# Kernel tuning notes

Hardware: AMD Instinct MI355X
Metric: run time of the kernel (lower is better)

## Reference

```python
import jax, jax.numpy as jnp
import numpy as np

B, N_GENES, N_SETS, G = 256, 10000, 1000, 128   # batch, input_dim, output_dim, geneset_size
H1, H2 = 64, 32                                  # hidden_dims
EPS = 1e-5                                       # BatchNorm1d eps


def _batchnorm(h, gamma, beta):
    # BatchNorm1d in training mode: biased batch stats over the batch axis
    mean = jnp.mean(h, axis=0, keepdims=True)
    var = jnp.mean(jnp.square(h - mean), axis=0, keepdims=True)
    return (h - mean) * jax.lax.rsqrt(var + EPS) * gamma + beta


def setup_inputs() -> dict:
    key = jax.random.key(0)
    ks = jax.random.split(key, 7)
    # Adjacency with exactly G distinct ones per column -> gather index list [N_SETS, G]
    rng = np.random.default_rng(0)
    gene_idx = np.argsort(rng.random((N_SETS, N_GENES)), axis=1)[:, :G]
    gene_idx = jnp.asarray(np.sort(gene_idx, axis=1), dtype=jnp.int32)

    x = jax.random.normal(ks[0], (B, N_GENES), jnp.float32)
    s1, s2, s3 = 1.0 / np.sqrt(G), 1.0 / np.sqrt(H1), 1.0 / np.sqrt(H2)
    W1 = jax.random.uniform(ks[1], (N_SETS, G, H1), jnp.float32, -s1, s1)
    b1 = jax.random.uniform(ks[2], (N_SETS, H1), jnp.float32, -s1, s1)
    W2 = jax.random.uniform(ks[3], (N_SETS, H1, H2), jnp.float32, -s2, s2)
    b2 = jax.random.uniform(ks[4], (N_SETS, H2), jnp.float32, -s2, s2)
    W3 = jax.random.uniform(ks[5], (N_SETS, H2), jnp.float32, -s3, s3)
    b3 = jax.random.uniform(ks[6], (N_SETS,), jnp.float32, -s3, s3)
    g1 = jnp.ones((N_SETS, H1), jnp.float32)
    be1 = jnp.zeros((N_SETS, H1), jnp.float32)
    g2 = jnp.ones((N_SETS, H2), jnp.float32)
    be2 = jnp.zeros((N_SETS, H2), jnp.float32)
    return {"x": x, "gene_idx": gene_idx, "W1": W1, "b1": b1, "g1": g1, "be1": be1,
            "W2": W2, "b2": b2, "g2": g2, "be2": be2, "W3": W3, "b3": b3}


def reference(x, gene_idx, W1, b1, g1, be1, W2, b2, g2, be2, W3, b3):
    # Per-geneset gather: x[:, adj[:,i]==1] for all i at once -> [B, S, G]
    xg = x[:, gene_idx]
    # Linear -> ReLU -> BatchNorm (per geneset, grouped GEMM)
    h = jax.nn.relu(jnp.einsum('bsg,sgh->bsh', xg, W1) + b1)
    h = _batchnorm(h, g1, be1)
    h = jax.nn.relu(jnp.einsum('bsh,shk->bsk', h, W2) + b2)
    h = _batchnorm(h, g2, be2)
    # Final Linear(H2 -> 1) -> ReLU, concatenated over genesets -> [B, S]
    out = jax.nn.relu(jnp.einsum('bsh,sh->bs', h, W3) + b3)
    return out
```

## Files before the change

### kernel.cpp

```cpp
#include <hip/hip_runtime.h>
#include <hip/hip_bf16.h>
#include <stdint.h>

#define BB 256
#define NG 10000
#define NS 1000
#define GG 128
#define H1 64
#define H2 32
#define EPSV 1e-5f


typedef unsigned short ushortT;
typedef __attribute__((ext_vector_type(4))) short short4v;
typedef __attribute__((ext_vector_type(8))) short short8v;
typedef __attribute__((ext_vector_type(4))) float float4v;

__device__ __forceinline__ float bf2f(ushortT u) {
    union { uint32_t i; float f; } v; v.i = ((uint32_t)u) << 16; return v.f;
}
__device__ __forceinline__ ushortT f2bf(float f) {
    union { __hip_bfloat16 h; ushortT u; } cv;
    cv.h = __float2bfloat16(f);
    return cv.u;
}
__device__ __forceinline__ uint32_t pack2(ushortT lo, ushortT hi) {
    return (uint32_t)lo | ((uint32_t)hi << 16);
}
__device__ __forceinline__ bool probe_f32(const void* g1) {
    return ((*(const uint32_t*)g1) & 0xFFFFu) == 0u;
}
__device__ __forceinline__ float loadf(const void* p, int i, bool isf) {
    return isf ? ((const float*)p)[i] : bf2f(((const ushortT*)p)[i]);
}
__device__ __forceinline__ ushortT loadbf(const void* p, size_t i, bool isf) {
    return isf ? f2bf(((const float*)p)[i]) : ((const ushortT*)p)[i];
}

__global__ __launch_bounds__(256) void k_transpose(const void* __restrict__ x,
                                                   ushortT* __restrict__ xT,
                                                   const void* __restrict__ g1p) {
    __shared__ ushortT tile[64][66];
    const bool isf = probe_f32(g1p);
    const int tx = threadIdx.x & 63;
    const int tz = threadIdx.x >> 6;
    const int j0 = blockIdx.x * 64;
    const int b0 = blockIdx.y * 64;
    const int j = j0 + tx;
#pragma unroll
    for (int k = 0; k < 16; ++k) {
        int bl = tz * 16 + k;
        ushortT v = 0;
        if (j < NG) v = loadbf(x, (size_t)(b0 + bl) * NG + j, isf);
        tile[bl][tx] = v;
    }
    __syncthreads();
#pragma unroll
    for (int k = 0; k < 16; ++k) {
        int jl = tz * 16 + k;
        int jw = j0 + jl;
        if (jw < NG) xT[jw * BB + b0 + tx] = tile[tx][jl];
    }
}

__global__ __launch_bounds__(256, 3) void k_main(
    const ushortT* __restrict__ xT, const int* __restrict__ gidx,
    const void* __restrict__ W1, const void* __restrict__ W2,
    const void* __restrict__ b1, const void* __restrict__ g1, const void* __restrict__ be1,
    const void* __restrict__ b2, const void* __restrict__ g2, const void* __restrict__ be2,
    const void* __restrict__ W3, const void* __restrict__ b3,
    void* __restrict__ out) {
    __shared__ ushortT xg[BB * 68];
    __shared__ ushortT w1s[2][64 * 36];

    char* xgc = (char*)xg;
    float* redf = (float*)w1s;
    ushortT* w2s = (ushortT*)w1s;

    const bool isf = probe_f32(g1);
    const int s = blockIdx.x;
    const int t = threadIdx.x;
    const int w = t >> 6;
    const int lane = t & 63;
    const int l16 = lane & 15;
    const int quad = lane >> 4;
    const size_t base1 = (size_t)s * (GG * H1);
    const size_t base2 = (size_t)s * (H1 * H2);

#define HOLEI(i)     (*(int*)(xgc + ((i) >> 1) * 136 + 128 + ((i) & 1) * 4))
#define HOLEF(r0, k) (*(float*)(xgc + ((r0) + ((k) >> 1)) * 136 + 128 + ((k) & 1) * 4))

    float b1v[4], w3v[2], b2v[2];
#pragma unroll
    for (int nt = 0; nt < 4; ++nt) b1v[nt] = loadf(b1, s * H1 + nt * 16 + l16, isf);
#pragma unroll
    for (int nt = 0; nt < 2; ++nt) {
        b2v[nt] = loadf(b2, s * H2 + nt * 16 + l16, isf);
        w3v[nt] = loadf(W3, s * H2 + nt * 16 + l16, isf);
    }
    const float b3v = loadf(b3, s, isf);
    float g1v = 0.f, be1v = 0.f, g2v = 0.f, be2v = 0.f;
    if (t < 64) { g1v = loadf(g1, s * H1 + t, isf); be1v = loadf(be1, s * H1 + t, isf); }
    if (t < 32) { g2v = loadf(g2, s * H2 + t, isf); be2v = loadf(be2, s * H2 + t, isf); }

    ushortT w2r[8];
    {
        const int k2 = t & 31, h0 = (t >> 5) * 8;
#pragma unroll
        for (int j = 0; j < 8; ++j) w2r[j] = loadbf(W2, base2 + (size_t)(h0 + j) * H2 + k2, isf);
    }

    if (t < GG) HOLEI(t) = gidx[s * GG + t];

    auto stageW1 = [&](int q, ushortT* dst) {
#pragma unroll
        for (int rep = 0; rep < 2; ++rep) {
            const int el = rep * 256 + t;
            const int e4 = q * 512 + el;
            const int g = el >> 4;
            const int h0 = (el & 15) * 4;
            ushortT u0, u1, u2, u3;
            if (isf) {
                float4 v = *(const float4*)((const float*)W1 + base1 + (size_t)e4 * 4);
                u0 = f2bf(v.x); u1 = f2bf(v.y); u2 = f2bf(v.z); u3 = f2bf(v.w);
            } else {
                uint2 v = *(const uint2*)((const ushortT*)W1 + base1 + (size_t)e4 * 4);
                u0 = (ushortT)v.x; u1 = (ushortT)(v.x >> 16);
                u2 = (ushortT)v.y; u3 = (ushortT)(v.y >> 16);
            }
            dst[(h0 + 0) * 36 + g] = u0;
            dst[(h0 + 1) * 36 + g] = u1;
            dst[(h0 + 2) * 36 + g] = u2;
            dst[(h0 + 3) * 36 + g] = u3;
        }
    };
    stageW1(0, w1s[0]);
    __syncthreads();

    float4v acc1[4][4];
#pragma unroll
    for (int mt = 0; mt < 4; ++mt)
#pragma unroll
        for (int nt = 0; nt < 4; ++nt) acc1[mt][nt] = (float4v){0.f, 0.f, 0.f, 0.f};

#pragma unroll
    for (int q = 0; q < 4; ++q) {
        if ((q & 1) == 0) {
            const int c = q >> 1;
#pragma unroll
            for (int gq = 0; gq < 8; ++gq) {
                const int i0 = c * 64 + gq * 8;
                int2 p0 = *(const int2*)(xgc + (i0 >> 1) * 136 + 128);
                int2 p1 = *(const int2*)(xgc + ((i0 >> 1) + 1) * 136 + 128);
                int2 p2 = *(const int2*)(xgc + ((i0 >> 1) + 2) * 136 + 128);
                int2 p3 = *(const int2*)(xgc + ((i0 >> 1) + 3) * 136 + 128);
                ushortT v0 = xT[p0.x * BB + t], v1 = xT[p0.y * BB + t];
                ushortT v2 = xT[p1.x * BB + t], v3 = xT[p1.y * BB + t];
                ushortT v4 = xT[p2.x * BB + t], v5 = xT[p2.y * BB + t];
                ushortT v6 = xT[p3.x * BB + t], v7 = xT[p3.y * BB + t];
                uint2 pa = {pack2(v0, v1), pack2(v2, v3)};
                uint2 pb = {pack2(v4, v5), pack2(v6, v7)};
                *(uint2*)(&xg[t * 68 + gq * 8]) = pa;
                *(uint2*)(&xg[t * 68 + gq * 8 + 4]) = pb;
            }
        }
        if (q < 3) stageW1(q + 1, w1s[(q + 1) & 1]);

        const ushortT* wbuf = w1s[q & 1];
        const int kt = q & 1;
        short8v bfrag[4];
#pragma unroll
        for (int nt = 0; nt < 4; ++nt) {
            const int h = nt * 16 + l16;
            const int woff = h * 36 + quad * 8;
            short4v blo = *(const short4v*)(&wbuf[woff]);
            short4v bhi = *(const short4v*)(&wbuf[woff + 4]);
            bfrag[nt] = __builtin_shufflevector(blo, bhi, 0, 1, 2, 3, 4, 5, 6, 7);
        }
#pragma unroll
        for (int mt = 0; mt < 4; ++mt) {
            const int b = w * 64 + mt * 16 + l16;
            const ushortT* p = &xg[b * 68 + kt * 32 + quad * 8];
            short4v alo = *(const short4v*)(p);
            short4v ahi = *(const short4v*)(p + 4);
            short8v af = __builtin_shufflevector(alo, ahi, 0, 1, 2, 3, 4, 5, 6, 7);
#pragma unroll
            for (int nt = 0; nt < 4; ++nt)
                acc1[mt][nt] = __builtin_amdgcn_mfma_f32_16x16x32_bf16(af, bfrag[nt], acc1[mt][nt], 0, 0, 0);
        }
        if (q < 3) __syncthreads();
    }

    float s1v[4], s2v[4];
#pragma unroll
    for (int nt = 0; nt < 4; ++nt) {
        float s1 = 0.f, s2 = 0.f;
        const float bb = b1v[nt];
#pragma unroll
        for (int mt = 0; mt < 4; ++mt)
#pragma unroll
            for (int r = 0; r < 4; ++r) {
                float v = acc1[mt][nt][r] + bb;
                v = v > 0.f ? v : 0.f;
                s1 += v;
                s2 += v * v;
            }
        s1 += __shfl_xor(s1, 16); s1 += __shfl_xor(s1, 32);
        s2 += __shfl_xor(s2, 16); s2 += __shfl_xor(s2, 32);
        s1v[nt] = s1; s2v[nt] = s2;
    }
    __syncthreads();
    if (lane < 16) {
#pragma unroll
        for (int nt = 0; nt < 4; ++nt) {
            const int k = w * 64 + nt * 16 + lane;
            redf[k] = s1v[nt];
            redf[256 + k] = s2v[nt];
        }
    }
    __syncthreads();

    if (t < 64) {
        float ts = redf[t] + redf[64 + t] + redf[128 + t] + redf[192 + t];
        float tq = redf[256 + t] + redf[320 + t] + redf[384 + t] + redf[448 + t];
        float mean = ts * (1.0f / 256.0f);
        float var = tq * (1.0f / 256.0f) - mean * mean;
        var = var > 0.f ? var : 0.f;
        float rs = rsqrtf(var + EPSV);
        float a = g1v * rs;
        HOLEF(64, t) = a;
        HOLEF(96, t) = be1v - mean * a;
    }
    __syncthreads();

    {
        const int k2 = t & 31, h0 = (t >> 5) * 8;
        uint4 pk;
        pk.x = pack2(w2r[0], w2r[1]);
        pk.y = pack2(w2r[2], w2r[3]);
        pk.z = pack2(w2r[4], w2r[5]);
        pk.w = pack2(w2r[6], w2r[7]);
        *(uint4*)(&w2s[k2 * 72 + h0]) = pk;
    }
#pragma unroll
    for (int nt = 0; nt < 4; ++nt) {
        const int h = nt * 16 + l16;
        const float bb = b1v[nt];
        const float a = HOLEF(64, h), cc = HOLEF(96, h);
#pragma unroll
        for (int mt = 0; mt < 4; ++mt)
#pragma unroll
            for (int r = 0; r < 4; ++r) {
                const int b = w * 64 + mt * 16 + quad * 4 + r;
                float v = acc1[mt][nt][r] + bb;
                v = v > 0.f ? v : 0.f;
                xg[b * 68 + h] = f2bf(v * a + cc);
            }
    }
    __syncthreads();

    float4v acc2[4][2];
#pragma unroll
    for (int mt = 0; mt < 4; ++mt)
#pragma unroll
        for (int nt = 0; nt < 2; ++nt) acc2[mt][nt] = (float4v){0.f, 0.f, 0.f, 0.f};

#pragma unroll
    for (int kt = 0; kt < 2; ++kt) {
        const int kl = kt * 32 + quad * 8;
        short8v bfrag2[2];
#pragma unroll
        for (int nt = 0; nt < 2; ++nt) {
            const int k2 = nt * 16 + l16;
            const int woff = k2 * 72 + kl;
            short4v blo = *(const short4v*)(&w2s[woff]);
            short4v bhi = *(const short4v*)(&w2s[woff + 4]);
            bfrag2[nt] = __builtin_shufflevector(blo, bhi, 0, 1, 2, 3, 4, 5, 6, 7);
        }
#pragma unroll
        for (int mt = 0; mt < 4; ++mt) {
            const int b = w * 64 + mt * 16 + l16;
            const ushortT* p = &xg[b * 68 + kl];
            short4v alo = *(const short4v*)(p);
            short4v ahi = *(const short4v*)(p + 4);
            short8v af = __builtin_shufflevector(alo, ahi, 0, 1, 2, 3, 4, 5, 6, 7);
#pragma unroll
            for (int nt = 0; nt < 2; ++nt)
                acc2[mt][nt] = __builtin_amdgcn_mfma_f32_16x16x32_bf16(af, bfrag2[nt], acc2[mt][nt], 0, 0, 0);
        }
    }

#pragma unroll
    for (int nt = 0; nt < 2; ++nt) {
        float s1 = 0.f, s2 = 0.f;
        const float bb = b2v[nt];
#pragma unroll
        for (int mt = 0; mt < 4; ++mt)
#pragma unroll
            for (int r = 0; r < 4; ++r) {
                float v = acc2[mt][nt][r] + bb;
                v = v > 0.f ? v : 0.f;
                s1 += v;
                s2 += v * v;
            }
        s1 += __shfl_xor(s1, 16); s1 += __shfl_xor(s1, 32);
        s2 += __shfl_xor(s2, 16); s2 += __shfl_xor(s2, 32);
        if (lane < 16) {
            const int k = w * 32 + nt * 16 + lane;
            HOLEF(0, k) = s1;
            HOLEF(64, k) = s2;
        }
    }
    __syncthreads();

    if (t < 32) {
        float ts = HOLEF(0, t) + HOLEF(0, 32 + t) + HOLEF(0, 64 + t) + HOLEF(0, 96 + t);
        float tq = HOLEF(64, t) + HOLEF(64, 32 + t) + HOLEF(64, 64 + t) + HOLEF(64, 96 + t);
        float mean = ts * (1.0f / 256.0f);
        float var = tq * (1.0f / 256.0f) - mean * mean;
        var = var > 0.f ? var : 0.f;
        float rs = rsqrtf(var + EPSV);
        float a = g2v * rs;
        HOLEF(128, t) = a;
        HOLEF(144, t) = be2v - mean * a;
    }
    __syncthreads();

    float a2[2], c2[2];
#pragma unroll
    for (int nt = 0; nt < 2; ++nt) {
        const int k2 = nt * 16 + l16;
        a2[nt] = HOLEF(128, k2);
        c2[nt] = HOLEF(144, k2);
    }
#pragma unroll
    for (int mt = 0; mt < 4; ++mt)
#pragma unroll
        for (int r = 0; r < 4; ++r) {
            float tot = 0.f;
#pragma unroll
            for (int nt = 0; nt < 2; ++nt) {
                float v = acc2[mt][nt][r] + b2v[nt];
                v = v > 0.f ? v : 0.f;
                tot += (v * a2[nt] + c2[nt]) * w3v[nt];
            }
            tot += __shfl_xor(tot, 1);
            tot += __shfl_xor(tot, 2);
            tot += __shfl_xor(tot, 4);
            tot += __shfl_xor(tot, 8);
            if (l16 == 0) {
                const int b = w * 64 + mt * 16 + quad * 4 + r;
                float o = tot + b3v;
                o = o > 0.f ? o : 0.f;
                if (isf) ((float*)out)[b * NS + s] = o;
                else     ((ushortT*)out)[b * NS + s] = f2bf(o);
            }
        }
#undef HOLEI
#undef HOLEF
}

extern "C" void kernel_launch(void* const* d_in, const int* in_sizes, int n_in,
                              void* d_out, int out_size, void* d_ws, size_t ws_size,
                              hipStream_t stream) {
    const int* gi = (const int*)d_in[1];
    ushortT* xT = (ushortT*)d_ws;

    dim3 gT((NG + 63) / 64, BB / 64);
    k_transpose<<<gT, 256, 0, stream>>>(d_in[0], xT, d_in[4]);
    k_main<<<NS, 256, 0, stream>>>(xT, gi, d_in[2], d_in[6],
                                   d_in[3], d_in[4], d_in[5],
                                   d_in[7], d_in[8], d_in[9], d_in[10], d_in[11],
                                   d_out);
}
```

Measured before the change: 152.3 us.

## Load GEMM1 operands directly from global into MFMA fragments, drop LDS staging

Replaces the LDS-staged gather of x and the double-buffered W1 staging with direct per-lane global loads into MFMA A/B fragments, templated on input dtype. This removes the barriers and LDS round trips inside the GEMM1 loop and frees shared memory, so occupancy is raised to 4 blocks per CU. The cost is many scalar 2-byte global loads per fragment: strided W1 reads and gathered xT reads that are not coalesced the way the staged path was, so memory efficiency may drop. It also merges the BN1 stats barrier and switches the GEMM2 fragment reads to element-wise loads.

New measurement: 173.8 us. +14.1%, slower.

```diff
diff --git a/kernel.cpp b/kernel.cpp
--- a/kernel.cpp
+++ b/kernel.cpp
@@ -12,7 +12,6 @@
 
 
 typedef unsigned short ushortT;
-typedef __attribute__((ext_vector_type(4))) short short4v;
 typedef __attribute__((ext_vector_type(8))) short short8v;
 typedef __attribute__((ext_vector_type(4))) float float4v;
 
@@ -63,19 +62,62 @@
     }
 }
 
-__global__ __launch_bounds__(256, 3) void k_main(
+template <bool ISF>
+__device__ __forceinline__ void run_gemm1(
+    const ushortT* __restrict__ xT, const void* __restrict__ W1, size_t base1,
+    const int* __restrict__ sIdxL, int w, int l16, int quad,
+    float4v (&acc1)[4][4]) {
+#pragma unroll
+    for (int q = 0; q < 4; ++q) {
+        int gg[8];
+#pragma unroll
+        for (int jj = 0; jj < 4; ++jj) {
+            int2 gp = *(const int2*)(&sIdxL[q * 32 + quad * 8 + jj * 2]);
+            gg[jj * 2] = gp.x;
+            gg[jj * 2 + 1] = gp.y;
+        }
+        short8v bfrag[4];
+#pragma unroll
+        for (int nt = 0; nt < 4; ++nt) {
+            const int h = nt * 16 + l16;
+            short8v bf;
+#pragma unroll
+            for (int j = 0; j < 8; ++j) {
+                const int gl = q * 32 + quad * 8 + j;
+                ushortT u;
+                if (ISF) u = f2bf(((const float*)W1)[base1 + (size_t)gl * H1 + h]);
+                else     u = ((const ushortT*)W1)[base1 + (size_t)gl * H1 + h];
+                bf[j] = (short)u;
+            }
+            bfrag[nt] = bf;
+        }
+#pragma unroll
+        for (int mt = 0; mt < 4; ++mt) {
+            const int b = w * 64 + mt * 16 + l16;
+            short8v af;
+#pragma unroll
+            for (int j = 0; j < 8; ++j) af[j] = (short)xT[(size_t)gg[j] * BB + b];
+#pragma unroll
+            for (int nt = 0; nt < 4; ++nt)
+                acc1[mt][nt] = __builtin_amdgcn_mfma_f32_16x16x32_bf16(af, bfrag[nt], acc1[mt][nt], 0, 0, 0);
+        }
+    }
+}
+
+__global__ __launch_bounds__(256, 4) void k_main(
     const ushortT* __restrict__ xT, const int* __restrict__ gidx,
     const void* __restrict__ W1, const void* __restrict__ W2,
     const void* __restrict__ b1, const void* __restrict__ g1, const void* __restrict__ be1,
     const void* __restrict__ b2, const void* __restrict__ g2, const void* __restrict__ be2,
     const void* __restrict__ W3, const void* __restrict__ b3,
     void* __restrict__ out) {
-    __shared__ ushortT xg[BB * 68];
-    __shared__ ushortT w1s[2][64 * 36];
-
-    char* xgc = (char*)xg;
-    float* redf = (float*)w1s;
-    ushortT* w2s = (ushortT*)w1s;
+    __shared__ ushortT h1s[BB * 68];
+    __shared__ ushortT arena[2304];
+    __shared__ int sIdxL[GG];
+
+    char* h1c = (char*)h1s;
+    float* redf = (float*)arena;
+    ushortT* w2s = arena;
 
     const bool isf = probe_f32(g1);
     const int s = blockIdx.x;
@@ -87,8 +129,7 @@
     const size_t base1 = (size_t)s * (GG * H1);
     const size_t base2 = (size_t)s * (H1 * H2);
 
-#define HOLEI(i)     (*(int*)(xgc + ((i) >> 1) * 136 + 128 + ((i) & 1) * 4))
-#define HOLEF(r0, k) (*(float*)(xgc + ((r0) + ((k) >> 1)) * 136 + 128 + ((k) & 1) * 4))
+#define HOLEF(r0, k) (*(float*)(h1c + ((r0) + ((k) >> 1)) * 136 + 128 + ((k) & 1) * 4))
 
     float b1v[4], w3v[2], b2v[2];
 #pragma unroll
@@ -110,31 +151,7 @@
         for (int j = 0; j < 8; ++j) w2r[j] = loadbf(W2, base2 + (size_t)(h0 + j) * H2 + k2, isf);
     }
 
-    if (t < GG) HOLEI(t) = gidx[s * GG + t];
-
-    auto stageW1 = [&](int q, ushortT* dst) {
-#pragma unroll
-        for (int rep = 0; rep < 2; ++rep) {
-            const int el = rep * 256 + t;
-            const int e4 = q * 512 + el;
-            const int g = el >> 4;
-            const int h0 = (el & 15) * 4;
-            ushortT u0, u1, u2, u3;
-            if (isf) {
-                float4 v = *(const float4*)((const float*)W1 + base1 + (size_t)e4 * 4);
-                u0 = f2bf(v.x); u1 = f2bf(v.y); u2 = f2bf(v.z); u3 = f2bf(v.w);
-            } else {
-                uint2 v = *(const uint2*)((const ushortT*)W1 + base1 + (size_t)e4 * 4);
-                u0 = (ushortT)v.x; u1 = (ushortT)(v.x >> 16);
-                u2 = (ushortT)v.y; u3 = (ushortT)(v.y >> 16);
-            }
-            dst[(h0 + 0) * 36 + g] = u0;
-            dst[(h0 + 1) * 36 + g] = u1;
-            dst[(h0 + 2) * 36 + g] = u2;
-            dst[(h0 + 3) * 36 + g] = u3;
-        }
-    };
-    stageW1(0, w1s[0]);
+    if (t < GG) sIdxL[t] = gidx[s * GG + t];
     __syncthreads();
 
     float4v acc1[4][4];
@@ -143,55 +160,9 @@
 #pragma unroll
         for (int nt = 0; nt < 4; ++nt) acc1[mt][nt] = (float4v){0.f, 0.f, 0.f, 0.f};
 
-#pragma unroll
-    for (int q = 0; q < 4; ++q) {
-        if ((q & 1) == 0) {
-            const int c = q >> 1;
-#pragma unroll
-            for (int gq = 0; gq < 8; ++gq) {
-                const int i0 = c * 64 + gq * 8;
-                int2 p0 = *(const int2*)(xgc + (i0 >> 1) * 136 + 128);
-                int2 p1 = *(const int2*)(xgc + ((i0 >> 1) + 1) * 136 + 128);
-                int2 p2 = *(const int2*)(xgc + ((i0 >> 1) + 2) * 136 + 128);
-                int2 p3 = *(const int2*)(xgc + ((i0 >> 1) + 3) * 136 + 128);
-                ushortT v0 = xT[p0.x * BB + t], v1 = xT[p0.y * BB + t];
-                ushortT v2 = xT[p1.x * BB + t], v3 = xT[p1.y * BB + t];
-                ushortT v4 = xT[p2.x * BB + t], v5 = xT[p2.y * BB + t];
-                ushortT v6 = xT[p3.x * BB + t], v7 = xT[p3.y * BB + t];
-                uint2 pa = {pack2(v0, v1), pack2(v2, v3)};
-                uint2 pb = {pack2(v4, v5), pack2(v6, v7)};
-                *(uint2*)(&xg[t * 68 + gq * 8]) = pa;
-                *(uint2*)(&xg[t * 68 + gq * 8 + 4]) = pb;
-            }
-        }
-        if (q < 3) stageW1(q + 1, w1s[(q + 1) & 1]);
-
-        const ushortT* wbuf = w1s[q & 1];
-        const int kt = q & 1;
-        short8v bfrag[4];
-#pragma unroll
-        for (int nt = 0; nt < 4; ++nt) {
-            const int h = nt * 16 + l16;
-            const int woff = h * 36 + quad * 8;
-            short4v blo = *(const short4v*)(&wbuf[woff]);
-            short4v bhi = *(const short4v*)(&wbuf[woff + 4]);
-            bfrag[nt] = __builtin_shufflevector(blo, bhi, 0, 1, 2, 3, 4, 5, 6, 7);
-        }
-#pragma unroll
-        for (int mt = 0; mt < 4; ++mt) {
-            const int b = w * 64 + mt * 16 + l16;
-            const ushortT* p = &xg[b * 68 + kt * 32 + quad * 8];
-            short4v alo = *(const short4v*)(p);
-            short4v ahi = *(const short4v*)(p + 4);
-            short8v af = __builtin_shufflevector(alo, ahi, 0, 1, 2, 3, 4, 5, 6, 7);
-#pragma unroll
-            for (int nt = 0; nt < 4; ++nt)
-                acc1[mt][nt] = __builtin_amdgcn_mfma_f32_16x16x32_bf16(af, bfrag[nt], acc1[mt][nt], 0, 0, 0);
-        }
-        if (q < 3) __syncthreads();
-    }
-
-    float s1v[4], s2v[4];
+    if (isf) run_gemm1<true>(xT, W1, base1, sIdxL, w, l16, quad, acc1);
+    else     run_gemm1<false>(xT, W1, base1, sIdxL, w, l16, quad, acc1);
+
 #pragma unroll
     for (int nt = 0; nt < 4; ++nt) {
         float s1 = 0.f, s2 = 0.f;
@@ -207,15 +178,10 @@
             }
         s1 += __shfl_xor(s1, 16); s1 += __shfl_xor(s1, 32);
         s2 += __shfl_xor(s2, 16); s2 += __shfl_xor(s2, 32);
-        s1v[nt] = s1; s2v[nt] = s2;
-    }
-    __syncthreads();
-    if (lane < 16) {
-#pragma unroll
-        for (int nt = 0; nt < 4; ++nt) {
+        if (lane < 16) {
             const int k = w * 64 + nt * 16 + lane;
-            redf[k] = s1v[nt];
-            redf[256 + k] = s2v[nt];
+            redf[k] = s1;
+            redf[256 + k] = s2;
         }
     }
     __syncthreads();
@@ -254,7 +220,7 @@
                 const int b = w * 64 + mt * 16 + quad * 4 + r;
                 float v = acc1[mt][nt][r] + bb;
                 v = v > 0.f ? v : 0.f;
-                xg[b * 68 + h] = f2bf(v * a + cc);
+                h1s[b * 68 + h] = f2bf(v * a + cc);
             }
     }
     __syncthreads();
@@ -272,18 +238,19 @@
 #pragma unroll
         for (int nt = 0; nt < 2; ++nt) {
             const int k2 = nt * 16 + l16;
-            const int woff = k2 * 72 + kl;
-            short4v blo = *(const short4v*)(&w2s[woff]);
-            short4v bhi = *(const short4v*)(&w2s[woff + 4]);
-            bfrag2[nt] = __builtin_shufflevector(blo, bhi, 0, 1, 2, 3, 4, 5, 6, 7);
+            const ushortT* p = &w2s[k2 * 72 + kl];
+            short8v bf;
+#pragma unroll
+            for (int j = 0; j < 8; ++j) bf[j] = (short)p[j];
+            bfrag2[nt] = bf;
         }
 #pragma unroll
         for (int mt = 0; mt < 4; ++mt) {
             const int b = w * 64 + mt * 16 + l16;
-            const ushortT* p = &xg[b * 68 + kl];
-            short4v alo = *(const short4v*)(p);
-            short4v ahi = *(const short4v*)(p + 4);
-            short8v af = __builtin_shufflevector(alo, ahi, 0, 1, 2, 3, 4, 5, 6, 7);
+            const ushortT* p = &h1s[b * 68 + kl];
+            short8v af;
+#pragma unroll
+            for (int j = 0; j < 8; ++j) af[j] = (short)p[j];
 #pragma unroll
             for (int nt = 0; nt < 2; ++nt)
                 acc2[mt][nt] = __builtin_amdgcn_mfma_f32_16x16x32_bf16(af, bfrag2[nt], acc2[mt][nt], 0, 0, 0);
@@ -356,7 +323,6 @@
                 else     ((ushortT*)out)[b * NS + s] = f2bf(o);
             }
         }
-#undef HOLEI
 #undef HOLEF
 }
 
```

## Single-buffer W1 in LDS via register staging and raise occupancy to four blocks

Applied to the files above, without the earlier changes.

Replaces the double-buffered W1 LDS tile with one buffer. The next W1 chunk is prefetched into registers during the MFMA loop and written to LDS between two barriers. This cuts LDS per block and raises the launch-bounds occupancy hint from three to four blocks per CU, so more work can hide gather latency. In exchange it adds a barrier per iteration and tighter register limits, which could cause spills.

Measured after the change: 144.6 us. 1.05x faster.

```diff
diff --git a/kernel.cpp b/kernel.cpp
--- a/kernel.cpp
+++ b/kernel.cpp
@@ -63,7 +63,7 @@
     }
 }
 
-__global__ __launch_bounds__(256, 3) void k_main(
+__global__ __launch_bounds__(256, 4) void k_main(
     const ushortT* __restrict__ xT, const int* __restrict__ gidx,
     const void* __restrict__ W1, const void* __restrict__ W2,
     const void* __restrict__ b1, const void* __restrict__ g1, const void* __restrict__ be1,
@@ -71,11 +71,11 @@
     const void* __restrict__ W3, const void* __restrict__ b3,
     void* __restrict__ out) {
     __shared__ ushortT xg[BB * 68];
-    __shared__ ushortT w1s[2][64 * 36];
+    __shared__ ushortT w1s[64 * 36];
 
     char* xgc = (char*)xg;
     float* redf = (float*)w1s;
-    ushortT* w2s = (ushortT*)w1s;
+    ushortT* w2s = w1s;
 
     const bool isf = probe_f32(g1);
     const int s = blockIdx.x;
@@ -112,29 +112,37 @@
 
     if (t < GG) HOLEI(t) = gidx[s * GG + t];
 
-    auto stageW1 = [&](int q, ushortT* dst) {
+    auto loadW1 = [&](int q, uint2* pk) {
+#pragma unroll
+        for (int rep = 0; rep < 2; ++rep) {
+            const int e4 = q * 512 + rep * 256 + t;
+            if (isf) {
+                float4 v = *(const float4*)((const float*)W1 + base1 + (size_t)e4 * 4);
+                pk[rep].x = pack2(f2bf(v.x), f2bf(v.y));
+                pk[rep].y = pack2(f2bf(v.z), f2bf(v.w));
+            } else {
+                pk[rep] = *(const uint2*)((const ushortT*)W1 + base1 + (size_t)e4 * 4);
+            }
+        }
+    };
+    auto writeW1 = [&](const uint2* pk) {
 #pragma unroll
         for (int rep = 0; rep < 2; ++rep) {
             const int el = rep * 256 + t;
-            const int e4 = q * 512 + el;
             const int g = el >> 4;
             const int h0 = (el & 15) * 4;
-            ushortT u0, u1, u2, u3;
-            if (isf) {
-                float4 v = *(const float4*)((const float*)W1 + base1 + (size_t)e4 * 4);
-                u0 = f2bf(v.x); u1 = f2bf(v.y); u2 = f2bf(v.z); u3 = f2bf(v.w);
-            } else {
-                uint2 v = *(const uint2*)((const ushortT*)W1 + base1 + (size_t)e4 * 4);
-                u0 = (ushortT)v.x; u1 = (ushortT)(v.x >> 16);
-                u2 = (ushortT)v.y; u3 = (ushortT)(v.y >> 16);
-            }
-            dst[(h0 + 0) * 36 + g] = u0;
-            dst[(h0 + 1) * 36 + g] = u1;
-            dst[(h0 + 2) * 36 + g] = u2;
-            dst[(h0 + 3) * 36 + g] = u3;
+            w1s[(h0 + 0) * 36 + g] = (ushortT)pk[rep].x;
+            w1s[(h0 + 1) * 36 + g] = (ushortT)(pk[rep].x >> 16);
+            w1s[(h0 + 2) * 36 + g] = (ushortT)pk[rep].y;
+            w1s[(h0 + 3) * 36 + g] = (ushortT)(pk[rep].y >> 16);
         }
     };
-    stageW1(0, w1s[0]);
+
+    {
+        uint2 pk0[2];
+        loadW1(0, pk0);
+        writeW1(pk0);
+    }
     __syncthreads();
 
     float4v acc1[4][4];
@@ -164,17 +172,17 @@
                 *(uint2*)(&xg[t * 68 + gq * 8 + 4]) = pb;
             }
         }
-        if (q < 3) stageW1(q + 1, w1s[(q + 1) & 1]);
-
-        const ushortT* wbuf = w1s[q & 1];
+        uint2 nxt[2];
+        if (q < 3) loadW1(q + 1, nxt);
+
         const int kt = q & 1;
         short8v bfrag[4];
 #pragma unroll
         for (int nt = 0; nt < 4; ++nt) {
             const int h = nt * 16 + l16;
             const int woff = h * 36 + quad * 8;
-            short4v blo = *(const short4v*)(&wbuf[woff]);
-            short4v bhi = *(const short4v*)(&wbuf[woff + 4]);
+            short4v blo = *(const short4v*)(&w1s[woff]);
+            short4v bhi = *(const short4v*)(&w1s[woff + 4]);
             bfrag[nt] = __builtin_shufflevector(blo, bhi, 0, 1, 2, 3, 4, 5, 6, 7);
         }
 #pragma unroll
@@ -188,7 +196,11 @@
             for (int nt = 0; nt < 4; ++nt)
                 acc1[mt][nt] = __builtin_amdgcn_mfma_f32_16x16x32_bf16(af, bfrag[nt], acc1[mt][nt], 0, 0, 0);
         }
-        if (q < 3) __syncthreads();
+        if (q < 3) {
+            __syncthreads();
+            writeW1(nxt);
+            __syncthreads();
+        }
     }
 
     float s1v[4], s2v[4];
```
